# Kernel optimization log

Measured on AMD Instinct MI355X. Metric: run time of the kernel, lower is better.

The kernel has to match this reference:

```python
import jax, jax.numpy as jnp
import numpy as np

D_MODEL = 256
D_STATE = 128          # d_model // 2
D_CONV = 4
EXPAND = 4
D_INNER = EXPAND * D_MODEL  # 1024
DT_RANK = (D_MODEL + 15) // 16  # 16
N_HEADS = 8
D_FF = 4 * D_MODEL
EPS = 1e-6


def layer_norm(x, a, b):
    # torch LayerNorm-like but with unbiased std (ddof=1) per the source
    mean = jnp.mean(x, axis=-1, keepdims=True)
    d = x.shape[-1]
    var = jnp.sum((x - mean) ** 2, axis=-1, keepdims=True) / (d - 1)
    std = jnp.sqrt(var)
    return a * (x - mean) / (std + EPS) + b


def silu(x):
    return x * jax.nn.sigmoid(x)


def mamba(x, in_proj_w, conv_w, conv_b, x_proj_w, dt_proj_w, dt_proj_b, A_log, Dp, out_proj_w):
    B, L, _ = x.shape
    xz = jnp.einsum('bld,ed->ble', x, in_proj_w)  # (B,L,2*D_INNER)
    xi, z = xz[..., :D_INNER], xz[..., D_INNER:]
    # causal depthwise conv1d over L
    xp = jnp.pad(xi, ((0, 0), (D_CONV - 1, 0), (0, 0)))
    u = conv_b
    for k in range(D_CONV):
        u = u + xp[:, k:k + L, :] * conv_w[:, k]
    u = silu(u)  # (B,L,D_INNER)
    dbl = jnp.einsum('bld,ed->ble', u, x_proj_w)  # (B,L,DT_RANK+2*D_STATE)
    dt = dbl[..., :DT_RANK]
    Bm = dbl[..., DT_RANK:DT_RANK + D_STATE]
    Cm = dbl[..., DT_RANK + D_STATE:]
    dt = jax.nn.softplus(jnp.einsum('blr,dr->bld', dt, dt_proj_w) + dt_proj_b)  # (B,L,D_INNER)
    A = -jnp.exp(A_log)  # (D_INNER, D_STATE)
    dA = jnp.exp(jnp.einsum('bld,dn->bldn', dt, A))          # (B,L,Din,N)
    dBu = jnp.einsum('bld,bln,bld->bldn', dt, Bm, u)          # (B,L,Din,N)

    def step(h, inp):
        dA_t, dBu_t, C_t = inp
        h = dA_t * h + dBu_t                    # (B,Din,N)
        y = jnp.einsum('bdn,bn->bd', h, C_t)    # (B,Din)
        return h, y

    h0 = jnp.zeros((B, D_INNER, D_STATE), dtype=x.dtype)
    _, ys = jax.lax.scan(step, h0, (jnp.swapaxes(dA, 0, 1), jnp.swapaxes(dBu, 0, 1), jnp.swapaxes(Cm, 0, 1)))
    y = jnp.swapaxes(ys, 0, 1) + u * Dp  # (B,L,Din)
    y = y * silu(z)
    return jnp.einsum('ble,de->bld', y, out_proj_w)


def cross_attention(q_in, kv_in, mask, wq_w, wq_b, wk_w, wk_b, wv_w, wv_b, wo_w, wo_b):
    B, Lq, _ = q_in.shape
    Lk = kv_in.shape[1]
    dk = D_MODEL // N_HEADS
    q = (jnp.einsum('bld,ed->ble', q_in, wq_w) + wq_b).reshape(B, Lq, N_HEADS, dk).transpose(0, 2, 1, 3)
    k = (jnp.einsum('bld,ed->ble', kv_in, wk_w) + wk_b).reshape(B, Lk, N_HEADS, dk).transpose(0, 2, 1, 3)
    v = (jnp.einsum('bld,ed->ble', kv_in, wv_w) + wv_b).reshape(B, Lk, N_HEADS, dk).transpose(0, 2, 1, 3)
    scores = jnp.einsum('bhqd,bhkd->bhqk', q, k) / np.sqrt(dk)
    # mask: (B,1,Lk) bool -> broadcast (B,1,1,Lk)
    scores = jnp.where(mask[:, None, :, :], scores, jnp.finfo(scores.dtype).min)
    p = jax.nn.softmax(scores, axis=-1)
    o = jnp.einsum('bhqk,bhkd->bhqd', p, v).transpose(0, 2, 1, 3).reshape(B, Lq, D_MODEL)
    return jnp.einsum('ble,de->bld', o, wo_w) + wo_b


def setup_inputs() -> dict:
    key = jax.random.key(0)
    ks = jax.random.split(key, 24)
    s = 0.02
    B, L, Lm = 2, 512, 512
    inp = {
        'x': jax.random.normal(ks[0], (B, L, D_MODEL), jnp.float32),
        'memory': jax.random.normal(ks[1], (B, Lm, D_MODEL), jnp.float32),
        'src_mask': jnp.ones((B, 1, Lm), bool),
        'tgt_mask': jnp.ones((B, 1, L), bool),
        # mamba params
        'in_proj_w': jax.random.normal(ks[2], (2 * D_INNER, D_MODEL)) * s,
        'conv_w': jax.random.normal(ks[3], (D_INNER, D_CONV)) * s,
        'conv_b': jnp.zeros((D_INNER,)),
        'x_proj_w': jax.random.normal(ks[4], (DT_RANK + 2 * D_STATE, D_INNER)) * s,
        'dt_proj_w': jax.random.normal(ks[5], (D_INNER, DT_RANK)) * s,
        'dt_proj_b': jnp.log(jnp.expm1(0.01)) * jnp.ones((D_INNER,)),
        'A_log': jnp.log(jnp.broadcast_to(jnp.arange(1, D_STATE + 1, dtype=jnp.float32), (D_INNER, D_STATE))),
        'Dp': jnp.ones((D_INNER,)),
        'out_proj_w': jax.random.normal(ks[6], (D_MODEL, D_INNER)) * s,
        # norms
        'norm1_a': jnp.ones((D_MODEL,)), 'norm1_b': jnp.zeros((D_MODEL,)),
        'norm2_a': jnp.ones((D_MODEL,)), 'norm2_b': jnp.zeros((D_MODEL,)),
        'norm3_a': jnp.ones((D_MODEL,)), 'norm3_b': jnp.zeros((D_MODEL,)),
        # cross attention
        'wq_w': jax.random.normal(ks[7], (D_MODEL, D_MODEL)) * s, 'wq_b': jnp.zeros((D_MODEL,)),
        'wk_w': jax.random.normal(ks[8], (D_MODEL, D_MODEL)) * s, 'wk_b': jnp.zeros((D_MODEL,)),
        'wv_w': jax.random.normal(ks[9], (D_MODEL, D_MODEL)) * s, 'wv_b': jnp.zeros((D_MODEL,)),
        'wo_w': jax.random.normal(ks[10], (D_MODEL, D_MODEL)) * s, 'wo_b': jnp.zeros((D_MODEL,)),
        # ffn
        'w1_w': jax.random.normal(ks[11], (D_FF, D_MODEL)) * s, 'w1_b': jnp.zeros((D_FF,)),
        'w2_w': jax.random.normal(ks[12], (D_MODEL, D_FF)) * s, 'w2_b': jnp.zeros((D_MODEL,)),
    }
    return inp


def reference(x, memory, src_mask, tgt_mask,
              in_proj_w, conv_w, conv_b, x_proj_w, dt_proj_w, dt_proj_b, A_log, Dp, out_proj_w,
              norm1_a, norm1_b, norm2_a, norm2_b, norm3_a, norm3_b,
              wq_w, wq_b, wk_w, wk_b, wv_w, wv_b, wo_w, wo_b,
              w1_w, w1_b, w2_w, w2_b):
    # self mamba block (pre-norm, residual); dropout = 0
    h = x + mamba(layer_norm(x, norm1_a, norm1_b), in_proj_w, conv_w, conv_b,
                  x_proj_w, dt_proj_w, dt_proj_b, A_log, Dp, out_proj_w)
    # cross attention block
    h = h + cross_attention(layer_norm(h, norm2_a, norm2_b), memory, src_mask,
                            wq_w, wq_b, wk_w, wk_b, wv_w, wv_b, wo_w, wo_b)
    # ffn block
    hn = layer_norm(h, norm3_a, norm3_b)
    ff = jnp.einsum('blf,df->bld', jax.nn.relu(jnp.einsum('bld,fd->blf', hn, w1_w) + w1_b), w2_w) + w2_b
    return h + ff
```

## Files before the change

kernel.cpp:

```cpp
#include <hip/hip_runtime.h>
#include <hip/hip_bf16.h>

#define B_SZ 2
#define L_SEQ 512
#define D_MODEL 256
#define D_STATE 128
#define D_CONV 4
#define D_INNER 1024
#define DT_RANK 16
#define N_HEADS 8
#define DK 32
#define D_FF 1024
#define R_TOT (B_SZ * L_SEQ)
#define DBL_LD (DT_RANK + 2 * D_STATE)
#define NSEG 16
#define SEGL 32
#define DPB 4

typedef __hip_bfloat16 bf16;
typedef __attribute__((ext_vector_type(8))) short short8;
typedef __attribute__((ext_vector_type(4))) float floatx4;

__device__ inline float fexp(float x) { return __expf(x); }
__device__ inline float fexp2(float x) { return __builtin_amdgcn_exp2f(x); }
__device__ inline float frcp(float x) { return __builtin_amdgcn_rcpf(x); }
__device__ inline float silu_f(float x) { return x * frcp(1.f + fexp(-x)); }
__device__ inline float softplus_f(float x) { return (x > 20.f) ? x : __logf(1.f + fexp(x)); }
__device__ inline float bf2f(unsigned short u) { return __uint_as_float(((unsigned)u) << 16); }

__device__ inline float swz_xor16(float x) {
    return __int_as_float(__builtin_amdgcn_ds_swizzle(__float_as_int(x), 0x401F));
}

#define S_MEM 262144
#define S_INW 524288
#define S_XPW 278528
#define S_OPW 262144
#define S_WQ  65536
#define S_WK  65536
#define S_WV  65536
#define S_WO  65536
#define S_W1  262144
#define S_W2  262144
#define S_TOT (S_MEM+S_INW+S_XPW+S_OPW+S_WQ+S_WK+S_WV+S_WO+S_W1+S_W2)
#define PACK_BLKS (S_TOT / 4 / 256)
#define Z1_F4 (R_TOT * D_MODEL / 4)
#define Z2_F4 (R_TOT * D_MODEL / 4)
#define Z3_F4 (R_TOT * DBL_LD / 4)
#define ZERO_BLKS ((Z1_F4 + Z2_F4 + Z3_F4 + 255) / 256)

__global__ __launch_bounds__(256) void pack_ln1(
    const float* __restrict__ s0, const float* __restrict__ s1,
    const float* __restrict__ s2, const float* __restrict__ s3,
    const float* __restrict__ s4, const float* __restrict__ s5,
    const float* __restrict__ s6, const float* __restrict__ s7,
    const float* __restrict__ s8, const float* __restrict__ s9,
    bf16* __restrict__ dst,
    const float* __restrict__ X, const float* __restrict__ a,
    const float* __restrict__ bvec, bf16* __restrict__ ln1b,
    float* __restrict__ zero1, float* __restrict__ zero2,
    float* __restrict__ zero3)
{
    __shared__ float r1[256], r2[256];
    if (blockIdx.x < PACK_BLKS) {
        const long e0 = ((long)blockIdx.x * 256 + threadIdx.x) * 4;
        const long off[11] = {0, S_MEM, S_MEM+S_INW, S_MEM+S_INW+S_XPW,
            S_MEM+S_INW+S_XPW+S_OPW, S_MEM+S_INW+S_XPW+S_OPW+S_WQ,
            S_MEM+S_INW+S_XPW+S_OPW+S_WQ+S_WK,
            S_MEM+S_INW+S_XPW+S_OPW+S_WQ+S_WK+S_WV,
            S_MEM+S_INW+S_XPW+S_OPW+S_WQ+S_WK+S_WV+S_WO,
            S_MEM+S_INW+S_XPW+S_OPW+S_WQ+S_WK+S_WV+S_WO+S_W1, S_TOT};
        const float* srcs[10] = {s0,s1,s2,s3,s4,s5,s6,s7,s8,s9};
        int seg = 0;
#pragma unroll
        for (int k = 1; k < 10; ++k) if (e0 >= off[k]) seg = k;
        const float4 v = *(const float4*)&srcs[seg][e0 - off[seg]];
        bf16 b0 = __float2bfloat16(v.x), b1 = __float2bfloat16(v.y);
        bf16 b2 = __float2bfloat16(v.z), b3 = __float2bfloat16(v.w);
        ushort4 pk;
        pk.x = *reinterpret_cast<unsigned short*>(&b0);
        pk.y = *reinterpret_cast<unsigned short*>(&b1);
        pk.z = *reinterpret_cast<unsigned short*>(&b2);
        pk.w = *reinterpret_cast<unsigned short*>(&b3);
        *reinterpret_cast<ushort4*>(dst + e0) = pk;
    } else if (blockIdx.x < PACK_BLKS + R_TOT) {
        const int row = blockIdx.x - PACK_BLKS;
        const int t = threadIdx.x;
        const float v = X[(long)row * D_MODEL + t];
        r1[t] = v;
        r2[t] = v * v;
        __syncthreads();
        for (int s = 128; s > 0; s >>= 1) {
            if (t < s) { r1[t] += r1[t + s]; r2[t] += r2[t + s]; }
            __syncthreads();
        }
        const float mean = r1[0] * (1.f / 256.f);
        const float var = (r2[0] - 256.f * mean * mean) * (1.f / 255.f);
        const float sd = sqrtf(fmaxf(var, 0.f));
        const float o = a[t] * (v - mean) / (sd + 1e-6f) + bvec[t];
        ln1b[(long)row * D_MODEL + t] = __float2bfloat16(o);
    } else {
        const long i4 = (long)(blockIdx.x - PACK_BLKS - R_TOT) * 256 + threadIdx.x;
        const float4 z = {0.f, 0.f, 0.f, 0.f};
        if (i4 < Z1_F4)                      *(float4*)&zero1[i4 * 4] = z;
        else if (i4 < Z1_F4 + Z2_F4)          *(float4*)&zero2[(i4 - Z1_F4) * 4] = z;
        else if (i4 < Z1_F4 + Z2_F4 + Z3_F4)  *(float4*)&zero3[(i4 - Z1_F4 - Z2_F4) * 4] = z;
    }
}

template <int EPI>
__global__ __launch_bounds__(256) void mfma_gemm(
    const bf16* __restrict__ A, const bf16* __restrict__ W, int K,
    float* __restrict__ C, bf16* __restrict__ Cb, int ldc,
    const float* __restrict__ bias, const float* __restrict__ res,
    int M, int N)
{
    const int wave = threadIdx.x >> 6;
    const int lane = threadIdx.x & 63;
    const int row16 = lane & 15;
    const int quad  = lane >> 4;
    const int bm = blockIdx.y * 64 + wave * 16;
    const int bn = blockIdx.x * 64;

    floatx4 acc[4];
#pragma unroll
    for (int t = 0; t < 4; ++t) acc[t] = (floatx4){0.f, 0.f, 0.f, 0.f};

    const long arow = (long)(bm + row16) * K;
    for (int k0 = 0; k0 < K; k0 += 32) {
        const short8 av = *(const short8*)(A + arow + k0 + quad * 8);
#pragma unroll
        for (int t = 0; t < 4; ++t) {
            const int gn = bn + t * 16 + row16;
            short8 bv = {0,0,0,0,0,0,0,0};
            if (gn < N) bv = *(const short8*)(W + (long)gn * K + k0 + quad * 8);
            acc[t] = __builtin_amdgcn_mfma_f32_16x16x32_bf16(av, bv, acc[t], 0, 0, 0);
        }
    }

#pragma unroll
    for (int t = 0; t < 4; ++t) {
        const int gn = bn + t * 16 + row16;
        if (gn >= N) continue;
        const float bs = bias ? bias[gn] : 0.f;
#pragma unroll
        for (int r = 0; r < 4; ++r) {
            const int gm = bm + quad * 4 + r;
            float v = acc[t][r] + bs;
            if (EPI == 1) v = fmaxf(v, 0.f);
            const long ci = (long)gm * ldc + gn;
            if (res) v += res[ci];
            if (C)  C[ci] = v;
            if (Cb) Cb[ci] = __float2bfloat16(v);
        }
    }
}

template <int SK>
__global__ __launch_bounds__(256) void splitk_gemm(
    const bf16* __restrict__ A, const bf16* __restrict__ W, int K,
    float* __restrict__ C, int ldc,
    const float* __restrict__ bias, const float* __restrict__ res,
    int M, int N)
{
    const int wave = threadIdx.x >> 6;
    const int lane = threadIdx.x & 63;
    const int row16 = lane & 15;
    const int quad  = lane >> 4;
    const int bm = blockIdx.y * 64 + wave * 16;
    const int bn = blockIdx.x * 64;
    const int kz = blockIdx.z;
    const int ksl = K / SK;
    const int kbeg = kz * ksl;

    floatx4 acc[4];
#pragma unroll
    for (int t = 0; t < 4; ++t) acc[t] = (floatx4){0.f, 0.f, 0.f, 0.f};

    const long arow = (long)(bm + row16) * K;
    for (int k0 = kbeg; k0 < kbeg + ksl; k0 += 32) {
        const short8 av = *(const short8*)(A + arow + k0 + quad * 8);
#pragma unroll
        for (int t = 0; t < 4; ++t) {
            const int gn = bn + t * 16 + row16;
            short8 bv = {0,0,0,0,0,0,0,0};
            if (gn < N) bv = *(const short8*)(W + (long)gn * K + k0 + quad * 8);
            acc[t] = __builtin_amdgcn_mfma_f32_16x16x32_bf16(av, bv, acc[t], 0, 0, 0);
        }
    }

#pragma unroll
    for (int t = 0; t < 4; ++t) {
        const int gn = bn + t * 16 + row16;
        if (gn >= N) continue;
        const float bs = (kz == 0 && bias) ? bias[gn] : 0.f;
#pragma unroll
        for (int r = 0; r < 4; ++r) {
            const int gm = bm + quad * 4 + r;
            float v = acc[t][r] + bs;
            const long ci = (long)gm * ldc + gn;
            if (kz == 0 && res) v += res[ci];
            atomicAdd(&C[ci], v);
        }
    }
}

__global__ __launch_bounds__(256) void xproj_kv_gemm(
    const bf16* __restrict__ ub, const bf16* __restrict__ XPWb,
    float* __restrict__ dbl,
    const bf16* __restrict__ memb, const bf16* __restrict__ WKb,
    const bf16* __restrict__ WVb,
    const float* __restrict__ WKB, const float* __restrict__ WVB,
    bf16* __restrict__ kbb, bf16* __restrict__ vbb)
{
    const int wave = threadIdx.x >> 6;
    const int lane = threadIdx.x & 63;
    const int row16 = lane & 15;
    const int quad  = lane >> 4;
    const int bm = blockIdx.y * 64 + wave * 16;
    const int bn = blockIdx.x * 64;
    const int z = blockIdx.z;

    floatx4 acc[4];
#pragma unroll
    for (int t = 0; t < 4; ++t) acc[t] = (floatx4){0.f, 0.f, 0.f, 0.f};

    if (z < 4) {
        const int K = D_INNER, N = DBL_LD;
        const int ksl = D_INNER / 4, kbeg = z * ksl;
        const long arow = (long)(bm + row16) * K;
        for (int k0 = kbeg; k0 < kbeg + ksl; k0 += 32) {
            const short8 av = *(const short8*)(ub + arow + k0 + quad * 8);
#pragma unroll
            for (int t = 0; t < 4; ++t) {
                const int gn = bn + t * 16 + row16;
                short8 bv = {0,0,0,0,0,0,0,0};
                if (gn < N) bv = *(const short8*)(XPWb + (long)gn * K + k0 + quad * 8);
                acc[t] = __builtin_amdgcn_mfma_f32_16x16x32_bf16(av, bv, acc[t], 0, 0, 0);
            }
        }
#pragma unroll
        for (int t = 0; t < 4; ++t) {
            const int gn = bn + t * 16 + row16;
            if (gn >= N) continue;
#pragma unroll
            for (int r = 0; r < 4; ++r) {
                const int gm = bm + quad * 4 + r;
                atomicAdd(&dbl[(long)gm * DBL_LD + gn], acc[t][r]);
            }
        }
    } else {
        if (bn >= D_MODEL) return;
        const int which = z - 4;
        const bf16* W = which ? WVb : WKb;
        const float* bias = which ? WVB : WKB;
        bf16* O = which ? vbb : kbb;
        const long arow = (long)(bm + row16) * D_MODEL;
        for (int k0 = 0; k0 < D_MODEL; k0 += 32) {
            const short8 av = *(const short8*)(memb + arow + k0 + quad * 8);
#pragma unroll
            for (int t = 0; t < 4; ++t) {
                const int gn = bn + t * 16 + row16;
                const short8 bv = *(const short8*)(W + (long)gn * D_MODEL + k0 + quad * 8);
                acc[t] = __builtin_amdgcn_mfma_f32_16x16x32_bf16(av, bv, acc[t], 0, 0, 0);
            }
        }
#pragma unroll
        for (int t = 0; t < 4; ++t) {
            const int gn = bn + t * 16 + row16;
            const float bs = bias[gn];
#pragma unroll
            for (int r = 0; r < 4; ++r) {
                const int gm = bm + quad * 4 + r;
                O[(long)gm * D_MODEL + gn] = __float2bfloat16(acc[t][r] + bs);
            }
        }
    }
}

__global__ __launch_bounds__(256) void gemm16_ln(
    const bf16* __restrict__ A, const bf16* __restrict__ W, int K,
    const float* __restrict__ bias, const float* __restrict__ res,
    float* __restrict__ Cf,
    const float* __restrict__ lna, const float* __restrict__ lnb,
    bf16* __restrict__ lnout)
{
    __shared__ float tile[16][264];
    __shared__ float red1[16][16];
    __shared__ float red2[16][16];
    const int w = threadIdx.x >> 6;
    const int lane = threadIdx.x & 63;
    const int row16 = lane & 15;
    const int quad  = lane >> 4;
    const int bm = blockIdx.x * 16;

    floatx4 acc[4];
#pragma unroll
    for (int t = 0; t < 4; ++t) acc[t] = (floatx4){0.f, 0.f, 0.f, 0.f};

    const long arow = (long)(bm + row16) * K;
    for (int k0 = 0; k0 < K; k0 += 32) {
        const short8 av = *(const short8*)(A + arow + k0 + quad * 8);
#pragma unroll
        for (int t = 0; t < 4; ++t) {
            const int gn = w * 64 + t * 16 + row16;
            const short8 bv = *(const short8*)(W + (long)gn * K + k0 + quad * 8);
            acc[t] = __builtin_amdgcn_mfma_f32_16x16x32_bf16(av, bv, acc[t], 0, 0, 0);
        }
    }

#pragma unroll
    for (int t = 0; t < 4; ++t) {
        const int gn = w * 64 + t * 16 + row16;
        const float bs = bias ? bias[gn] : 0.f;
#pragma unroll
        for (int r = 0; r < 4; ++r) {
            const int gm = bm + quad * 4 + r;
            float v = acc[t][r] + bs;
            const long ci = (long)gm * D_MODEL + gn;
            if (res) v += res[ci];
            Cf[ci] = v;
            tile[quad * 4 + r][gn] = v;
        }
    }
    __syncthreads();

    const int r = threadIdx.x >> 4;
    const int g = threadIdx.x & 15;
    float s = 0.f, q = 0.f;
#pragma unroll
    for (int i = 0; i < 16; ++i) {
        const float x = tile[r][g * 16 + i];
        s += x; q += x * x;
    }
    red1[r][g] = s; red2[r][g] = q;
    __syncthreads();
    float ts = 0.f, tq = 0.f;
#pragma unroll
    for (int i = 0; i < 16; ++i) { ts += red1[r][i]; tq += red2[r][i]; }
    const float mean = ts * (1.f / 256.f);
    const float var = (tq - 256.f * mean * mean) * (1.f / 255.f);
    const float sd = sqrtf(fmaxf(var, 0.f));
    const long rowbase = (long)(bm + r) * D_MODEL;
#pragma unroll
    for (int i = 0; i < 16; ++i) {
        const int c = g * 16 + i;
        const float o = lna[c] * (tile[r][c] - mean) / (sd + 1e-6f) + lnb[c];
        lnout[rowbase + c] = __float2bfloat16(o);
    }
}

__global__ __launch_bounds__(256) void ln_kernel(
    const float* __restrict__ x, const float* __restrict__ a,
    const float* __restrict__ bvec, bf16* __restrict__ out)
{
    const int row = blockIdx.x * 4 + (threadIdx.x >> 6);
    const int lane = threadIdx.x & 63;
    const float4 v = *(const float4*)&x[((long)row << 8) + lane * 4];
    float s = v.x + v.y + v.z + v.w;
    float q = fmaf(v.x, v.x, fmaf(v.y, v.y, fmaf(v.z, v.z, v.w * v.w)));
#pragma unroll
    for (int off = 32; off > 0; off >>= 1) {
        s += __shfl_xor(s, off, 64);
        q += __shfl_xor(q, off, 64);
    }
    const float mean = s * (1.f / 256.f);
    const float var = (q - 256.f * mean * mean) * (1.f / 255.f);
    const float sd = sqrtf(fmaxf(var, 0.f));
    const float4 a4 = *(const float4*)&a[lane * 4];
    const float4 b4 = *(const float4*)&bvec[lane * 4];
    const float o0 = a4.x * (v.x - mean) / (sd + 1e-6f) + b4.x;
    const float o1 = a4.y * (v.y - mean) / (sd + 1e-6f) + b4.y;
    const float o2 = a4.z * (v.z - mean) / (sd + 1e-6f) + b4.z;
    const float o3 = a4.w * (v.w - mean) / (sd + 1e-6f) + b4.w;
    bf16 c0 = __float2bfloat16(o0), c1 = __float2bfloat16(o1);
    bf16 c2 = __float2bfloat16(o2), c3 = __float2bfloat16(o3);
    ushort4 pk;
    pk.x = *reinterpret_cast<unsigned short*>(&c0);
    pk.y = *reinterpret_cast<unsigned short*>(&c1);
    pk.z = *reinterpret_cast<unsigned short*>(&c2);
    pk.w = *reinterpret_cast<unsigned short*>(&c3);
    *reinterpret_cast<ushort4*>(out + ((long)row << 8) + lane * 4) = pk;
}

__global__ __launch_bounds__(256) void conv_silu_T(
    const bf16* __restrict__ xz, const float* __restrict__ cw,
    const float* __restrict__ cb, bf16* __restrict__ ub, float* __restrict__ uT)
{
    __shared__ float t[64][65];
    const int db = blockIdx.x;
    const int lb = blockIdx.y;
    const int b  = blockIdx.z;
    const int tid = threadIdx.x;
    const int r  = tid >> 4;
    const int c4 = (tid & 15) * 4;
    const int d0 = db * 64 + c4;

    const float4 cb4 = *(const float4*)&cb[d0];
    float cwa[4][4];
#pragma unroll
    for (int i = 0; i < 4; ++i) {
        const float4 w = *(const float4*)&cw[(d0 + i) * 4];
        cwa[i][0] = w.x; cwa[i][1] = w.y; cwa[i][2] = w.z; cwa[i][3] = w.w;
    }

#pragma unroll
    for (int q = 0; q < 4; ++q) {
        const int ll = r + q * 16;
        const int l = lb * 64 + ll;
        float s0 = cb4.x, s1 = cb4.y, s2 = cb4.z, s3 = cb4.w;
#pragma unroll
        for (int k = 0; k < D_CONV; ++k) {
            const int ls = l - 3 + k;
            if (ls >= 0) {
                const ushort4 xv = *(const ushort4*)&xz[((long)(b * L_SEQ + ls)) * (2 * D_INNER) + d0];
                s0 = fmaf(bf2f(xv.x), cwa[0][k], s0);
                s1 = fmaf(bf2f(xv.y), cwa[1][k], s1);
                s2 = fmaf(bf2f(xv.z), cwa[2][k], s2);
                s3 = fmaf(bf2f(xv.w), cwa[3][k], s3);
            }
        }
        s0 = silu_f(s0); s1 = silu_f(s1); s2 = silu_f(s2); s3 = silu_f(s3);
        bf16 b0 = __float2bfloat16(s0), b1 = __float2bfloat16(s1);
        bf16 b2 = __float2bfloat16(s2), b3 = __float2bfloat16(s3);
        ushort4 pk;
        pk.x = *reinterpret_cast<unsigned short*>(&b0);
        pk.y = *reinterpret_cast<unsigned short*>(&b1);
        pk.z = *reinterpret_cast<unsigned short*>(&b2);
        pk.w = *reinterpret_cast<unsigned short*>(&b3);
        *reinterpret_cast<ushort4*>(ub + ((long)(b * L_SEQ + l)) * D_INNER + d0) = pk;
        t[c4 + 0][ll] = s0; t[c4 + 1][ll] = s1;
        t[c4 + 2][ll] = s2; t[c4 + 3][ll] = s3;
    }
    __syncthreads();
#pragma unroll
    for (int q = 0; q < 4; ++q) {
        const int dl = r + q * 16;
        float4 v = {t[dl][c4], t[dl][c4 + 1], t[dl][c4 + 2], t[dl][c4 + 3]};
        *(float4*)&uT[((long)(b * D_INNER + db * 64 + dl) << 9) + lb * 64 + c4] = v;
    }
}

__global__ __launch_bounds__(1024) void scan_fused(
    const float* __restrict__ uT,
    const float* __restrict__ dbl, const float* __restrict__ A_log,
    const float* __restrict__ DTW, const float* __restrict__ DTB,
    const float* __restrict__ Dp, const bf16* __restrict__ xz,
    bf16* __restrict__ yb)
{
    const int b  = blockIdx.x >> 8;
    const int d0 = (blockIdx.x & 255) * DPB;
    const int w = threadIdx.x >> 6;
    const int lane = threadIdx.x & 63;
    const int n0 = lane * 2;

    __shared__ float Sh[NSEG][DPB][D_STATE];
    __shared__ float Ph[NSEG][DPB][D_STATE];
    __shared__ float DtS[NSEG][DPB][SEGL];

    {
        const int dij = lane >> 4;
        const int ll  = (lane & 15) * 2;
        const int l   = w * SEGL + ll;
        const float* dr0 = dbl + (long)(b * L_SEQ + l) * DBL_LD;
        const float* dr1 = dr0 + DBL_LD;
        const float* wr  = DTW + (long)(d0 + dij) * DT_RANK;
        const float bs = DTB[d0 + dij];
        float a0 = 0.f, a1 = 0.f;
#pragma unroll
        for (int k = 0; k < DT_RANK; ++k) {
            const float wv = wr[k];
            a0 = fmaf(dr0[k], wv, a0);
            a1 = fmaf(dr1[k], wv, a1);
        }
        DtS[w][dij][ll]     = softplus_f(a0 + bs);
        DtS[w][dij][ll + 1] = softplus_f(a1 + bs);
    }

    float An0[DPB], An1[DPB];
#pragma unroll
    for (int di = 0; di < DPB; ++di) {
        An0[di] = -fexp(A_log[(long)(d0 + di) * D_STATE + n0]) * 1.44269504f;
        An1[di] = -fexp(A_log[(long)(d0 + di) * D_STATE + n0 + 1]) * 1.44269504f;
    }
    const float4 dp4 = *(const float4*)&Dp[d0];
    const float dpc[4] = {dp4.x, dp4.y, dp4.z, dp4.w};

    const float* blp = dbl + ((long)(b * L_SEQ + w * SEGL)) * DBL_LD + DT_RANK + n0;
    const float* clp = blp + D_STATE;
    const long tbase = ((long)(b * D_INNER + d0) << 9) + w * SEGL;

    if (w < NSEG - 1) {
        float h0[DPB] = {}, h1[DPB] = {}, sdt[DPB] = {};
        for (int s = 0; s < SEGL / 4; ++s) {
            float2 Bv[4];
#pragma unroll
            for (int j = 0; j < 4; ++j)
                Bv[j] = *(const float2*)(blp + (long)(s * 4 + j) * DBL_LD);
#pragma unroll
            for (int di = 0; di < DPB; ++di) {
                const float4 dt0 = *(const float4*)&DtS[w][di][s * 4];
                const float4 u0  = *(const float4*)(uT  + tbase + ((long)di << 9) + s * 4);
                const float dts[4] = {dt0.x, dt0.y, dt0.z, dt0.w};
                const float us[4]  = {u0.x, u0.y, u0.z, u0.w};
#pragma unroll
                for (int j = 0; j < 4; ++j) {
                    const float dtv = dts[j];
                    sdt[di] += dtv;
                    const float dtu = dtv * us[j];
                    h0[di] = fmaf(fexp2(dtv * An0[di]), h0[di], dtu * Bv[j].x);
                    h1[di] = fmaf(fexp2(dtv * An1[di]), h1[di], dtu * Bv[j].y);
                }
            }
        }
#pragma unroll
        for (int di = 0; di < DPB; ++di) {
            Sh[w][di][n0]     = h0[di];
            Sh[w][di][n0 + 1] = h1[di];
            Ph[w][di][n0]     = fexp2(An0[di] * sdt[di]);
            Ph[w][di][n0 + 1] = fexp2(An1[di] * sdt[di]);
        }
    }
    __syncthreads();

    float h0[DPB] = {}, h1[DPB] = {};
    for (int s = 0; s < w; ++s) {
#pragma unroll
        for (int di = 0; di < DPB; ++di) {
            h0[di] = fmaf(Ph[s][di][n0],     h0[di], Sh[s][di][n0]);
            h1[di] = fmaf(Ph[s][di][n0 + 1], h1[di], Sh[s][di][n0 + 1]);
        }
    }

    const int bpa = (lane ^ 32) << 2;
    const bool lo32 = lane < 32;
    const bool b16 = (lane & 16) != 0;
    const int g = lane >> 4;
    const bool wl = (lane & 15) == 15;

    for (int s = 0; s < SEGL / 4; ++s) {
        float2 Bv[4], Cv[4];
#pragma unroll
        for (int j = 0; j < 4; ++j) {
            Bv[j] = *(const float2*)(blp + (long)(s * 4 + j) * DBL_LD);
            Cv[j] = *(const float2*)(clp + (long)(s * 4 + j) * DBL_LD);
        }
        float zsel[DPB];
#pragma unroll
        for (int di = 0; di < DPB; ++di) {
            const float4 dt0 = *(const float4*)&DtS[w][di][s * 4];
            const float4 u0  = *(const float4*)(uT  + tbase + ((long)di << 9) + s * 4);
            const float dts[4] = {dt0.x, dt0.y, dt0.z, dt0.w};
            const float us[4]  = {u0.x, u0.y, u0.z, u0.w};
            float yp[4];
#pragma unroll
            for (int j = 0; j < 4; ++j) {
                const float dtv = dts[j];
                const float dtu = dtv * us[j];
                h0[di] = fmaf(fexp2(dtv * An0[di]), h0[di], dtu * Bv[j].x);
                h1[di] = fmaf(fexp2(dtv * An1[di]), h1[di], dtu * Bv[j].y);
                yp[j] = fmaf(h0[di], Cv[j].x, h1[di] * Cv[j].y);
            }
            if (lane == 0) {
#pragma unroll
                for (int j = 0; j < 4; ++j)
                    yp[j] = fmaf(us[j], dpc[di], yp[j]);
            }
            float z0[2];
#pragma unroll
            for (int j = 0; j < 2; ++j) {
                const float t = lo32 ? yp[j]     : yp[j + 2];
                const float u = lo32 ? yp[j + 2] : yp[j];
                z0[j] = t + __int_as_float(
                    __builtin_amdgcn_ds_bpermute(bpa, __float_as_int(u)));
            }
            float z2;
            {
                const float t = b16 ? z0[1] : z0[0];
                const float u = b16 ? z0[0] : z0[1];
                z2 = t + swz_xor16(u);
            }
            z2 += __int_as_float(__builtin_amdgcn_update_dpp(0, __float_as_int(z2), 0x111, 0xf, 0xf, true));
            z2 += __int_as_float(__builtin_amdgcn_update_dpp(0, __float_as_int(z2), 0x112, 0xf, 0xf, true));
            z2 += __int_as_float(__builtin_amdgcn_update_dpp(0, __float_as_int(z2), 0x114, 0xf, 0xf, true));
            z2 += __int_as_float(__builtin_amdgcn_update_dpp(0, __float_as_int(z2), 0x118, 0xf, 0xf, true));
            zsel[di] = z2;
        }
        if (wl) {
            const int l = w * SEGL + s * 4 + g;
            const long row = (long)b * L_SEQ + l;
            const ushort4 zu = *(const ushort4*)&xz[row * (2 * D_INNER) + D_INNER + d0];
            const float y0 = zsel[0] * silu_f(bf2f(zu.x));
            const float y1 = zsel[1] * silu_f(bf2f(zu.y));
            const float y2 = zsel[2] * silu_f(bf2f(zu.z));
            const float y3 = zsel[3] * silu_f(bf2f(zu.w));
            bf16 o0 = __float2bfloat16(y0), o1 = __float2bfloat16(y1);
            bf16 o2 = __float2bfloat16(y2), o3 = __float2bfloat16(y3);
            ushort4 pk;
            pk.x = *reinterpret_cast<unsigned short*>(&o0);
            pk.y = *reinterpret_cast<unsigned short*>(&o1);
            pk.z = *reinterpret_cast<unsigned short*>(&o2);
            pk.w = *reinterpret_cast<unsigned short*>(&o3);
            *reinterpret_cast<ushort4*>(yb + row * D_INNER + d0) = pk;
        }
    }
}

#define QT 16
#define CK 64

__global__ __launch_bounds__(256) void attn_kernel(
    const bf16* __restrict__ ln2b, const bf16* __restrict__ WQb,
    const float* __restrict__ WQB,
    const bf16* __restrict__ kbb, const bf16* __restrict__ vbb,
    bf16* __restrict__ o)
{
    const int qt = blockIdx.x;
    const int hh = blockIdx.y;
    const int b  = blockIdx.z;
    const int t = threadIdx.x;

    __shared__ float qs[QT][33];
    __shared__ float Ks[CK][36];
    __shared__ float Vs[CK][36];

    {
        const int qr = t >> 4;
        const int c  = (t * 2) & 31;
        const bf16* ar = ln2b + ((long)(b * L_SEQ + qt * QT + qr)) * D_MODEL;
        const bf16* w0 = WQb + (long)(hh * DK + c) * D_MODEL;
        const bf16* w1 = w0 + D_MODEL;
        float a0 = 0.f, a1 = 0.f;
        for (int kk = 0; kk < D_MODEL; kk += 8) {
            const short8 av = *(const short8*)(ar + kk);
            const short8 b0 = *(const short8*)(w0 + kk);
            const short8 b1 = *(const short8*)(w1 + kk);
#pragma unroll
            for (int e = 0; e < 8; ++e) {
                const float af = bf2f((unsigned short)av[e]);
                a0 = fmaf(af, bf2f((unsigned short)b0[e]), a0);
                a1 = fmaf(af, bf2f((unsigned short)b1[e]), a1);
            }
        }
        qs[qr][c]     = a0 + WQB[hh * DK + c];
        qs[qr][c + 1] = a1 + WQB[hh * DK + c + 1];
    }
    __syncthreads();

    const int lane = t & 15;
    const int qa = t >> 4;
    const int q0 = qt * QT + qa;
    const float scale = 0.17677669529663687f;
    float qr0[32];
#pragma unroll
    for (int i = 0; i < 32; ++i) qr0[i] = qs[qa][i] * scale;

    float m0 = -1e30f, l0 = 0.f, o0[32] = {};

    for (int c = 0; c < L_SEQ; c += CK) {
        __syncthreads();
        {
            const int row = t >> 2;
            const int c0  = (t & 3) * 8;
            const long base = (long)(b * L_SEQ + c + row) * D_MODEL + hh * DK + c0;
            const short8 k8 = *(const short8*)(kbb + base);
            const short8 v8 = *(const short8*)(vbb + base);
            float4 f;
            f.x = bf2f((unsigned short)k8[0]); f.y = bf2f((unsigned short)k8[1]);
            f.z = bf2f((unsigned short)k8[2]); f.w = bf2f((unsigned short)k8[3]);
            *(float4*)&Ks[row][c0] = f;
            f.x = bf2f((unsigned short)k8[4]); f.y = bf2f((unsigned short)k8[5]);
            f.z = bf2f((unsigned short)k8[6]); f.w = bf2f((unsigned short)k8[7]);
            *(float4*)&Ks[row][c0 + 4] = f;
            f.x = bf2f((unsigned short)v8[0]); f.y = bf2f((unsigned short)v8[1]);
            f.z = bf2f((unsigned short)v8[2]); f.w = bf2f((unsigned short)v8[3]);
            *(float4*)&Vs[row][c0] = f;
            f.x = bf2f((unsigned short)v8[4]); f.y = bf2f((unsigned short)v8[5]);
            f.z = bf2f((unsigned short)v8[6]); f.w = bf2f((unsigned short)v8[7]);
            *(float4*)&Vs[row][c0 + 4] = f;
        }
        __syncthreads();

        float s0[4];
#pragma unroll
        for (int i = 0; i < 4; ++i) {
            const int kk = i * 16 + lane;
            float a0 = 0.f;
#pragma unroll
            for (int dd = 0; dd < 32; dd += 4) {
                const float4 kv = *(const float4*)&Ks[kk][dd];
                a0 = fmaf(qr0[dd+0], kv.x, a0); a0 = fmaf(qr0[dd+1], kv.y, a0);
                a0 = fmaf(qr0[dd+2], kv.z, a0); a0 = fmaf(qr0[dd+3], kv.w, a0);
            }
            s0[i] = a0;
        }

        float cm0 = s0[0];
#pragma unroll
        for (int i = 1; i < 4; ++i) cm0 = fmaxf(cm0, s0[i]);
#pragma unroll
        for (int off = 8; off > 0; off >>= 1)
            cm0 = fmaxf(cm0, __shfl_down(cm0, off, 16));
        cm0 = __shfl(cm0, 0, 16);

        const float nm0 = fmaxf(m0, cm0);
        const float al0 = fexp(m0 - nm0);
        l0 *= al0;
#pragma unroll
        for (int dd = 0; dd < 32; ++dd) o0[dd] *= al0;
        m0 = nm0;

        float p0[4];
#pragma unroll
        for (int i = 0; i < 4; ++i) { p0[i] = fexp(s0[i] - m0); l0 += p0[i]; }

#pragma unroll
        for (int i = 0; i < 4; ++i) {
            const int kk = i * 16 + lane;
#pragma unroll
            for (int dd = 0; dd < 32; dd += 4) {
                const float4 vv = *(const float4*)&Vs[kk][dd];
                o0[dd+0] = fmaf(p0[i], vv.x, o0[dd+0]);
                o0[dd+1] = fmaf(p0[i], vv.y, o0[dd+1]);
                o0[dd+2] = fmaf(p0[i], vv.z, o0[dd+2]);
                o0[dd+3] = fmaf(p0[i], vv.w, o0[dd+3]);
            }
        }
    }

#pragma unroll
    for (int off = 8; off > 0; off >>= 1) {
        l0 += __shfl_down(l0, off, 16);
#pragma unroll
        for (int dd = 0; dd < 32; ++dd) o0[dd] += __shfl_down(o0[dd], off, 16);
    }
    if (lane == 0) {
        const float i0 = 1.f / l0;
        bf16* op0 = o + ((long)(b * L_SEQ + q0) * D_MODEL + hh * DK);
#pragma unroll
        for (int dd = 0; dd < 32; ++dd) op0[dd] = __float2bfloat16(o0[dd] * i0);
    }
}


extern "C" void kernel_launch(void* const* d_in, const int* in_sizes, int n_in,
                              void* d_out, int out_size, void* d_ws, size_t ws_size,
                              hipStream_t stream) {
    const float* X   = (const float*)d_in[0];
    const float* MEM = (const float*)d_in[1];
    const float* CW  = (const float*)d_in[5];
    const float* CB  = (const float*)d_in[6];
    const float* DTW = (const float*)d_in[8];
    const float* DTB = (const float*)d_in[9];
    const float* ALG = (const float*)d_in[10];
    const float* DP  = (const float*)d_in[11];
    const float* N1A = (const float*)d_in[13];
    const float* N1B = (const float*)d_in[14];
    const float* N2A = (const float*)d_in[15];
    const float* N2B = (const float*)d_in[16];
    const float* N3A = (const float*)d_in[17];
    const float* N3B = (const float*)d_in[18];
    const float* WQB = (const float*)d_in[20];
    const float* WKB = (const float*)d_in[22];
    const float* WVB = (const float*)d_in[24];
    const float* WOB = (const float*)d_in[26];
    const float* W1B = (const float*)d_in[28];
    const float* W2B = (const float*)d_in[30];
    const float* INW = (const float*)d_in[4];
    const float* XPW = (const float*)d_in[7];
    const float* OPW = (const float*)d_in[12];
    const float* WQ  = (const float*)d_in[19];
    const float* WKw = (const float*)d_in[21];
    const float* WVw = (const float*)d_in[23];
    const float* WO  = (const float*)d_in[25];
    const float* W1  = (const float*)d_in[27];
    const float* W2  = (const float*)d_in[29];
    float* out = (float*)d_out;

    bf16* bp = (bf16*)d_ws;
    bf16* ub   = bp;  bp += (long)R_TOT * D_INNER;
    bf16* ybb  = bp;  bp += (long)R_TOT * D_INNER;
    bf16* ffab = ybb;
    bf16* xzb  = bp;  bp += (long)R_TOT * 2 * D_INNER;
    bf16* ln1b = bp;  bp += (long)R_TOT * D_MODEL;
    bf16* aob  = ln1b;
    bf16* ln2b = bp;  bp += (long)R_TOT * D_MODEL;
    bf16* ln3b = ln2b;
    bf16* kbb  = bp;  bp += (long)R_TOT * D_MODEL;
    bf16* vbb  = bp;  bp += (long)R_TOT * D_MODEL;
    bf16* arena = bp; bp += S_TOT;
    bf16* MEMb = arena;
    bf16* INWb = MEMb + S_MEM;
    bf16* XPWb = INWb + S_INW;
    bf16* OPWb = XPWb + S_XPW;
    bf16* WQb  = OPWb + S_OPW;
    bf16* WKb  = WQb + S_WQ;
    bf16* WVb  = WKb + S_WK;
    bf16* WOb  = WVb + S_WV;
    bf16* W1b  = WOb + S_WO;
    bf16* W2b  = W1b + S_W1;

    float* p = (float*)(bp + ((((long)(bp - (bf16*)d_ws)) & 1) ? 1 : 0));
    float* uT  = p;                                  p += (long)R_TOT * D_INNER;
    float* dbl = p;                                  p += (long)R_TOT * DBL_LD;
    float* h1  = p;                                  p += (long)R_TOT * D_MODEL;
    float* h2  = p;                                  p += (long)R_TOT * D_MODEL;

    const dim3 blk256(256);
    const int MT64 = R_TOT / 64;

    pack_ln1<<<PACK_BLKS + R_TOT + ZERO_BLKS, blk256, 0, stream>>>(
        MEM, INW, XPW, OPW, WQ, WKw, WVw, WO, W1, W2, arena,
        X, N1A, N1B, ln1b, h1, out, dbl);

    mfma_gemm<0><<<dim3(2 * D_INNER / 64, MT64), blk256, 0, stream>>>(
        ln1b, INWb, D_MODEL, nullptr, xzb, 2 * D_INNER, nullptr, nullptr,
        R_TOT, 2 * D_INNER);

    conv_silu_T<<<dim3(D_INNER / 64, L_SEQ / 64, B_SZ), blk256, 0, stream>>>(
        xzb, CW, CB, ub, uT);

    xproj_kv_gemm<<<dim3((DBL_LD + 63) / 64, MT64, 6), blk256, 0, stream>>>(
        ub, XPWb, dbl, MEMb, WKb, WVb, WKB, WVB, kbb, vbb);

    scan_fused<<<B_SZ * D_INNER / DPB, dim3(1024), 0, stream>>>(
        uT, dbl, ALG, DTW, DTB, DP, xzb, ybb);

    splitk_gemm<4><<<dim3(D_MODEL / 64, MT64, 4), blk256, 0, stream>>>(
        ybb, OPWb, D_INNER, h1, D_MODEL, nullptr, X, R_TOT, D_MODEL);

    ln_kernel<<<R_TOT / 4, blk256, 0, stream>>>(h1, N2A, N2B, ln2b);

    attn_kernel<<<dim3(L_SEQ / QT, N_HEADS, B_SZ), blk256, 0, stream>>>(
        ln2b, WQb, WQB, kbb, vbb, aob);

    gemm16_ln<<<R_TOT / 16, blk256, 0, stream>>>(
        aob, WOb, D_MODEL, WOB, h1, h2, N3A, N3B, ln3b);

    mfma_gemm<1><<<dim3(D_FF / 64, MT64), blk256, 0, stream>>>(
        ln3b, W1b, D_MODEL, nullptr, ffab, D_FF, W1B, nullptr, R_TOT, D_FF);

    splitk_gemm<4><<<dim3(D_MODEL / 64, MT64, 4), blk256, 0, stream>>>(
        ffab, W2b, D_FF, out, D_MODEL, W2B, h2, R_TOT, D_MODEL);

    (void)in_sizes; (void)n_in; (void)out_size; (void)ws_size;
}
```

Baseline: 322.1 us.

## Fuse K/V projection into in_proj GEMM and LN2 into attention

Moves the memory K/V projection out of the x_proj split-K launch and into the in_proj GEMM launch as 8 extra column blocks, so x_proj runs with a smaller grid. The separate LayerNorm-2 kernel is removed and its work is recomputed inside each attention block, which normalizes its 16 query rows into shared memory before the Q projection. This saves one launch and the ln2 round trip through global memory, but the norm is now recomputed once per head (8x redundant), and the in_proj launch becomes slightly unbalanced. A helper for bf16 bit packing is also added as a cleanup.

```diff
diff --git a/kernel.cpp b/kernel.cpp
--- a/kernel.cpp
+++ b/kernel.cpp
@@ -27,6 +27,10 @@
 __device__ inline float silu_f(float x) { return x * frcp(1.f + fexp(-x)); }
 __device__ inline float softplus_f(float x) { return (x > 20.f) ? x : __logf(1.f + fexp(x)); }
 __device__ inline float bf2f(unsigned short u) { return __uint_as_float(((unsigned)u) << 16); }
+__device__ inline unsigned short f2bfbits(float x) {
+    bf16 h = __float2bfloat16(x);
+    return *reinterpret_cast<unsigned short*>(&h);
+}
 
 __device__ inline float swz_xor16(float x) {
     return __int_as_float(__builtin_amdgcn_ds_swizzle(__float_as_int(x), 0x401F));
@@ -75,13 +79,9 @@
 #pragma unroll
         for (int k = 1; k < 10; ++k) if (e0 >= off[k]) seg = k;
         const float4 v = *(const float4*)&srcs[seg][e0 - off[seg]];
-        bf16 b0 = __float2bfloat16(v.x), b1 = __float2bfloat16(v.y);
-        bf16 b2 = __float2bfloat16(v.z), b3 = __float2bfloat16(v.w);
         ushort4 pk;
-        pk.x = *reinterpret_cast<unsigned short*>(&b0);
-        pk.y = *reinterpret_cast<unsigned short*>(&b1);
-        pk.z = *reinterpret_cast<unsigned short*>(&b2);
-        pk.w = *reinterpret_cast<unsigned short*>(&b3);
+        pk.x = f2bfbits(v.x); pk.y = f2bfbits(v.y);
+        pk.z = f2bfbits(v.z); pk.w = f2bfbits(v.w);
         *reinterpret_cast<ushort4*>(dst + e0) = pk;
     } else if (blockIdx.x < PACK_BLKS + R_TOT) {
         const int row = blockIdx.x - PACK_BLKS;
@@ -105,6 +105,61 @@
         if (i4 < Z1_F4)                      *(float4*)&zero1[i4 * 4] = z;
         else if (i4 < Z1_F4 + Z2_F4)          *(float4*)&zero2[(i4 - Z1_F4) * 4] = z;
         else if (i4 < Z1_F4 + Z2_F4 + Z3_F4)  *(float4*)&zero3[(i4 - Z1_F4 - Z2_F4) * 4] = z;
+    }
+}
+
+__global__ __launch_bounds__(256) void xz_kv_gemm(
+    const bf16* __restrict__ ln1b, const bf16* __restrict__ INWb,
+    bf16* __restrict__ xzb,
+    const bf16* __restrict__ memb, const bf16* __restrict__ WKb,
+    const bf16* __restrict__ WVb,
+    const float* __restrict__ WKB, const float* __restrict__ WVB,
+    bf16* __restrict__ kbb, bf16* __restrict__ vbb)
+{
+    const int wave = threadIdx.x >> 6;
+    const int lane = threadIdx.x & 63;
+    const int row16 = lane & 15;
+    const int quad  = lane >> 4;
+    const int bm = blockIdx.y * 64 + wave * 16;
+    const int x = blockIdx.x;
+
+    const bf16* A; const bf16* W; const float* bias; bf16* O;
+    int bn, ldc;
+    if (x < 32) {
+        A = ln1b; W = INWb; bias = nullptr; O = xzb;
+        bn = x * 64; ldc = 2 * D_INNER;
+    } else {
+        const int e = x - 32;
+        const int which = e >> 2;
+        A = memb; W = which ? WVb : WKb; bias = which ? WVB : WKB;
+        O = which ? vbb : kbb;
+        bn = (e & 3) * 64; ldc = D_MODEL;
+    }
+
+    floatx4 acc[4];
+#pragma unroll
+    for (int t = 0; t < 4; ++t) acc[t] = (floatx4){0.f, 0.f, 0.f, 0.f};
+
+    const long arow = (long)(bm + row16) * D_MODEL;
+    for (int k0 = 0; k0 < D_MODEL; k0 += 32) {
+        const short8 av = *(const short8*)(A + arow + k0 + quad * 8);
+#pragma unroll
+        for (int t = 0; t < 4; ++t) {
+            const int gn = bn + t * 16 + row16;
+            const short8 bv = *(const short8*)(W + (long)gn * D_MODEL + k0 + quad * 8);
+            acc[t] = __builtin_amdgcn_mfma_f32_16x16x32_bf16(av, bv, acc[t], 0, 0, 0);
+        }
+    }
+
+#pragma unroll
+    for (int t = 0; t < 4; ++t) {
+        const int gn = bn + t * 16 + row16;
+        const float bs = bias ? bias[gn] : 0.f;
+#pragma unroll
+        for (int r = 0; r < 4; ++r) {
+            const int gm = bm + quad * 4 + r;
+            O[(long)gm * ldc + gn] = __float2bfloat16(acc[t][r] + bs);
+        }
     }
 }
 
@@ -205,13 +260,9 @@
     }
 }
 
-__global__ __launch_bounds__(256) void xproj_kv_gemm(
+__global__ __launch_bounds__(256) void xproj_gemm(
     const bf16* __restrict__ ub, const bf16* __restrict__ XPWb,
-    float* __restrict__ dbl,
-    const bf16* __restrict__ memb, const bf16* __restrict__ WKb,
-    const bf16* __restrict__ WVb,
-    const float* __restrict__ WKB, const float* __restrict__ WVB,
-    bf16* __restrict__ kbb, bf16* __restrict__ vbb)
+    float* __restrict__ dbl)
 {
     const int wave = threadIdx.x >> 6;
     const int lane = threadIdx.x & 63;
@@ -220,60 +271,32 @@
     const int bm = blockIdx.y * 64 + wave * 16;
     const int bn = blockIdx.x * 64;
     const int z = blockIdx.z;
+    const int ksl = D_INNER / 4, kbeg = z * ksl;
 
     floatx4 acc[4];
 #pragma unroll
     for (int t = 0; t < 4; ++t) acc[t] = (floatx4){0.f, 0.f, 0.f, 0.f};
 
-    if (z < 4) {
-        const int K = D_INNER, N = DBL_LD;
-        const int ksl = D_INNER / 4, kbeg = z * ksl;
-        const long arow = (long)(bm + row16) * K;
-        for (int k0 = kbeg; k0 < kbeg + ksl; k0 += 32) {
-            const short8 av = *(const short8*)(ub + arow + k0 + quad * 8);
-#pragma unroll
-            for (int t = 0; t < 4; ++t) {
-                const int gn = bn + t * 16 + row16;
-                short8 bv = {0,0,0,0,0,0,0,0};
-                if (gn < N) bv = *(const short8*)(XPWb + (long)gn * K + k0 + quad * 8);
-                acc[t] = __builtin_amdgcn_mfma_f32_16x16x32_bf16(av, bv, acc[t], 0, 0, 0);
-            }
-        }
+    const long arow = (long)(bm + row16) * D_INNER;
+    for (int k0 = kbeg; k0 < kbeg + ksl; k0 += 32) {
+        const short8 av = *(const short8*)(ub + arow + k0 + quad * 8);
 #pragma unroll
         for (int t = 0; t < 4; ++t) {
             const int gn = bn + t * 16 + row16;
-            if (gn >= N) continue;
-#pragma unroll
-            for (int r = 0; r < 4; ++r) {
-                const int gm = bm + quad * 4 + r;
-                atomicAdd(&dbl[(long)gm * DBL_LD + gn], acc[t][r]);
-            }
-        }
-    } else {
-        if (bn >= D_MODEL) return;
-        const int which = z - 4;
-        const bf16* W = which ? WVb : WKb;
-        const float* bias = which ? WVB : WKB;
-        bf16* O = which ? vbb : kbb;
-        const long arow = (long)(bm + row16) * D_MODEL;
-        for (int k0 = 0; k0 < D_MODEL; k0 += 32) {
-            const short8 av = *(const short8*)(memb + arow + k0 + quad * 8);
-#pragma unroll
-            for (int t = 0; t < 4; ++t) {
-                const int gn = bn + t * 16 + row16;
-                const short8 bv = *(const short8*)(W + (long)gn * D_MODEL + k0 + quad * 8);
-                acc[t] = __builtin_amdgcn_mfma_f32_16x16x32_bf16(av, bv, acc[t], 0, 0, 0);
-            }
-        }
-#pragma unroll
-        for (int t = 0; t < 4; ++t) {
-            const int gn = bn + t * 16 + row16;
-            const float bs = bias[gn];
-#pragma unroll
-            for (int r = 0; r < 4; ++r) {
-                const int gm = bm + quad * 4 + r;
-                O[(long)gm * D_MODEL + gn] = __float2bfloat16(acc[t][r] + bs);
-            }
+            short8 bv = {0,0,0,0,0,0,0,0};
+            if (gn < DBL_LD) bv = *(const short8*)(XPWb + (long)gn * D_INNER + k0 + quad * 8);
+            acc[t] = __builtin_amdgcn_mfma_f32_16x16x32_bf16(av, bv, acc[t], 0, 0, 0);
+        }
+    }
+
+#pragma unroll
+    for (int t = 0; t < 4; ++t) {
+        const int gn = bn + t * 16 + row16;
+        if (gn >= DBL_LD) continue;
+#pragma unroll
+        for (int r = 0; r < 4; ++r) {
+            const int gm = bm + quad * 4 + r;
+            atomicAdd(&dbl[(long)gm * DBL_LD + gn], acc[t][r]);
         }
     }
 }
@@ -350,39 +373,6 @@
     }
 }
 
-__global__ __launch_bounds__(256) void ln_kernel(
-    const float* __restrict__ x, const float* __restrict__ a,
-    const float* __restrict__ bvec, bf16* __restrict__ out)
-{
-    const int row = blockIdx.x * 4 + (threadIdx.x >> 6);
-    const int lane = threadIdx.x & 63;
-    const float4 v = *(const float4*)&x[((long)row << 8) + lane * 4];
-    float s = v.x + v.y + v.z + v.w;
-    float q = fmaf(v.x, v.x, fmaf(v.y, v.y, fmaf(v.z, v.z, v.w * v.w)));
-#pragma unroll
-    for (int off = 32; off > 0; off >>= 1) {
-        s += __shfl_xor(s, off, 64);
-        q += __shfl_xor(q, off, 64);
-    }
-    const float mean = s * (1.f / 256.f);
-    const float var = (q - 256.f * mean * mean) * (1.f / 255.f);
-    const float sd = sqrtf(fmaxf(var, 0.f));
-    const float4 a4 = *(const float4*)&a[lane * 4];
-    const float4 b4 = *(const float4*)&bvec[lane * 4];
-    const float o0 = a4.x * (v.x - mean) / (sd + 1e-6f) + b4.x;
-    const float o1 = a4.y * (v.y - mean) / (sd + 1e-6f) + b4.y;
-    const float o2 = a4.z * (v.z - mean) / (sd + 1e-6f) + b4.z;
-    const float o3 = a4.w * (v.w - mean) / (sd + 1e-6f) + b4.w;
-    bf16 c0 = __float2bfloat16(o0), c1 = __float2bfloat16(o1);
-    bf16 c2 = __float2bfloat16(o2), c3 = __float2bfloat16(o3);
-    ushort4 pk;
-    pk.x = *reinterpret_cast<unsigned short*>(&c0);
-    pk.y = *reinterpret_cast<unsigned short*>(&c1);
-    pk.z = *reinterpret_cast<unsigned short*>(&c2);
-    pk.w = *reinterpret_cast<unsigned short*>(&c3);
-    *reinterpret_cast<ushort4*>(out + ((long)row << 8) + lane * 4) = pk;
-}
-
 __global__ __launch_bounds__(256) void conv_silu_T(
     const bf16* __restrict__ xz, const float* __restrict__ cw,
     const float* __restrict__ cb, bf16* __restrict__ ub, float* __restrict__ uT)
@@ -421,13 +411,9 @@
             }
         }
         s0 = silu_f(s0); s1 = silu_f(s1); s2 = silu_f(s2); s3 = silu_f(s3);
-        bf16 b0 = __float2bfloat16(s0), b1 = __float2bfloat16(s1);
-        bf16 b2 = __float2bfloat16(s2), b3 = __float2bfloat16(s3);
         ushort4 pk;
-        pk.x = *reinterpret_cast<unsigned short*>(&b0);
-        pk.y = *reinterpret_cast<unsigned short*>(&b1);
-        pk.z = *reinterpret_cast<unsigned short*>(&b2);
-        pk.w = *reinterpret_cast<unsigned short*>(&b3);
+        pk.x = f2bfbits(s0); pk.y = f2bfbits(s1);
+        pk.z = f2bfbits(s2); pk.w = f2bfbits(s3);
         *reinterpret_cast<ushort4*>(ub + ((long)(b * L_SEQ + l)) * D_INNER + d0) = pk;
         t[c4 + 0][ll] = s0; t[c4 + 1][ll] = s1;
         t[c4 + 2][ll] = s2; t[c4 + 3][ll] = s3;
@@ -590,17 +576,11 @@
             const int l = w * SEGL + s * 4 + g;
             const long row = (long)b * L_SEQ + l;
             const ushort4 zu = *(const ushort4*)&xz[row * (2 * D_INNER) + D_INNER + d0];
-            const float y0 = zsel[0] * silu_f(bf2f(zu.x));
-            const float y1 = zsel[1] * silu_f(bf2f(zu.y));
-            const float y2 = zsel[2] * silu_f(bf2f(zu.z));
-            const float y3 = zsel[3] * silu_f(bf2f(zu.w));
-            bf16 o0 = __float2bfloat16(y0), o1 = __float2bfloat16(y1);
-            bf16 o2 = __float2bfloat16(y2), o3 = __float2bfloat16(y3);
             ushort4 pk;
-            pk.x = *reinterpret_cast<unsigned short*>(&o0);
-            pk.y = *reinterpret_cast<unsigned short*>(&o1);
-            pk.z = *reinterpret_cast<unsigned short*>(&o2);
-            pk.w = *reinterpret_cast<unsigned short*>(&o3);
+            pk.x = f2bfbits(zsel[0] * silu_f(bf2f(zu.x)));
+            pk.y = f2bfbits(zsel[1] * silu_f(bf2f(zu.y)));
+            pk.z = f2bfbits(zsel[2] * silu_f(bf2f(zu.z)));
+            pk.w = f2bfbits(zsel[3] * silu_f(bf2f(zu.w)));
             *reinterpret_cast<ushort4*>(yb + row * D_INNER + d0) = pk;
         }
     }
@@ -610,8 +590,9 @@
 #define CK 64
 
 __global__ __launch_bounds__(256) void attn_kernel(
-    const bf16* __restrict__ ln2b, const bf16* __restrict__ WQb,
-    const float* __restrict__ WQB,
+    const float* __restrict__ h1, const float* __restrict__ n2a,
+    const float* __restrict__ n2b,
+    const bf16* __restrict__ WQb, const float* __restrict__ WQB,
     const bf16* __restrict__ kbb, const bf16* __restrict__ vbb,
     bf16* __restrict__ o)
 {
@@ -620,14 +601,47 @@
     const int b  = blockIdx.z;
     const int t = threadIdx.x;
 
+    __shared__ unsigned short qln[QT][256];
     __shared__ float qs[QT][33];
     __shared__ float Ks[CK][36];
     __shared__ float Vs[CK][36];
 
     {
+        const int r  = t >> 4;
+        const int cg = (t & 15) * 16;
+        const long rb = ((long)(b * L_SEQ + qt * QT + r)) << 8;
+        float xv[16];
+        float s = 0.f, q = 0.f;
+#pragma unroll
+        for (int i = 0; i < 16; i += 4) {
+            const float4 v = *(const float4*)&h1[rb + cg + i];
+            xv[i] = v.x; xv[i+1] = v.y; xv[i+2] = v.z; xv[i+3] = v.w;
+            s += v.x + v.y + v.z + v.w;
+            q = fmaf(v.x, v.x, fmaf(v.y, v.y, fmaf(v.z, v.z, fmaf(v.w, v.w, q))));
+        }
+#pragma unroll
+        for (int off = 8; off > 0; off >>= 1) {
+            s += __shfl_xor(s, off, 16);
+            q += __shfl_xor(q, off, 16);
+        }
+        const float mean = s * (1.f / 256.f);
+        const float var = (q - 256.f * mean * mean) * (1.f / 255.f);
+        const float sd = sqrtf(fmaxf(var, 0.f));
+#pragma unroll
+        for (int i = 0; i < 16; i += 2) {
+            const int c = cg + i;
+            const float o0 = n2a[c]   * (xv[i]   - mean) / (sd + 1e-6f) + n2b[c];
+            const float o1 = n2a[c+1] * (xv[i+1] - mean) / (sd + 1e-6f) + n2b[c+1];
+            const unsigned int pk = (unsigned)f2bfbits(o0) | ((unsigned)f2bfbits(o1) << 16);
+            *(unsigned int*)&qln[r][c] = pk;
+        }
+    }
+    __syncthreads();
+
+    {
         const int qr = t >> 4;
         const int c  = (t * 2) & 31;
-        const bf16* ar = ln2b + ((long)(b * L_SEQ + qt * QT + qr)) * D_MODEL;
+        const bf16* ar = (const bf16*)&qln[qr][0];
         const bf16* w0 = WQb + (long)(hh * DK + c) * D_MODEL;
         const bf16* w1 = w0 + D_MODEL;
         float a0 = 0.f, a1 = 0.f;
@@ -784,8 +798,7 @@
     bf16* xzb  = bp;  bp += (long)R_TOT * 2 * D_INNER;
     bf16* ln1b = bp;  bp += (long)R_TOT * D_MODEL;
     bf16* aob  = ln1b;
-    bf16* ln2b = bp;  bp += (long)R_TOT * D_MODEL;
-    bf16* ln3b = ln2b;
+    bf16* ln3b = bp;  bp += (long)R_TOT * D_MODEL;
     bf16* kbb  = bp;  bp += (long)R_TOT * D_MODEL;
     bf16* vbb  = bp;  bp += (long)R_TOT * D_MODEL;
     bf16* arena = bp; bp += S_TOT;
@@ -813,15 +826,14 @@
         MEM, INW, XPW, OPW, WQ, WKw, WVw, WO, W1, W2, arena,
         X, N1A, N1B, ln1b, h1, out, dbl);
 
-    mfma_gemm<0><<<dim3(2 * D_INNER / 64, MT64), blk256, 0, stream>>>(
-        ln1b, INWb, D_MODEL, nullptr, xzb, 2 * D_INNER, nullptr, nullptr,
-        R_TOT, 2 * D_INNER);
+    xz_kv_gemm<<<dim3(40, MT64), blk256, 0, stream>>>(
+        ln1b, INWb, xzb, MEMb, WKb, WVb, WKB, WVB, kbb, vbb);
 
     conv_silu_T<<<dim3(D_INNER / 64, L_SEQ / 64, B_SZ), blk256, 0, stream>>>(
         xzb, CW, CB, ub, uT);
 
-    xproj_kv_gemm<<<dim3((DBL_LD + 63) / 64, MT64, 6), blk256, 0, stream>>>(
-        ub, XPWb, dbl, MEMb, WKb, WVb, WKB, WVB, kbb, vbb);
+    xproj_gemm<<<dim3((DBL_LD + 63) / 64, MT64, 4), blk256, 0, stream>>>(
+        ub, XPWb, dbl);
 
     scan_fused<<<B_SZ * D_INNER / DPB, dim3(1024), 0, stream>>>(
         uT, dbl, ALG, DTW, DTB, DP, xzb, ybb);
@@ -829,10 +841,8 @@
     splitk_gemm<4><<<dim3(D_MODEL / 64, MT64, 4), blk256, 0, stream>>>(
         ybb, OPWb, D_INNER, h1, D_MODEL, nullptr, X, R_TOT, D_MODEL);
 
-    ln_kernel<<<R_TOT / 4, blk256, 0, stream>>>(h1, N2A, N2B, ln2b);
-
     attn_kernel<<<dim3(L_SEQ / QT, N_HEADS, B_SZ), blk256, 0, stream>>>(
-        ln2b, WQb, WQB, kbb, vbb, aob);
+        h1, N2A, N2B, WQb, WQB, kbb, vbb, aob);
 
     gemm16_ln<<<R_TOT / 16, blk256, 0, stream>>>(
         aob, WOb, D_MODEL, WOB, h1, h2, N3A, N3B, ln3b);
```

Measured after the change: 322.7 us. No clear change (+0.2%).
